# Kernel optimization log

Hardware: AMD Instinct MI355X
Metric: run time of the kernel (lower is better)

The kernel has to match this reference:

```python
import jax, jax.numpy as jnp
import numpy as np

N = 65536          # particles
E = 524288         # relations (avg degree 8)
RIG = 4096         # rigid instance = particles [0, RIG); fluid = [RIG, N)
PSTEPS = 2
ATTR, STATE, RELD, NF = 3, 6, 1, 128
DT = 1.0 / 60.0
MEAN_P = np.zeros(3, np.float32); STD_P = np.ones(3, np.float32)
MEAN_V = np.zeros(3, np.float32); STD_V = np.ones(3, np.float32)


def _lin(x, w, b):
    return x @ w.T + b  # torch Linear convention: w is [out, in]


def setup_inputs() -> dict:
    key = jax.random.key(0)
    ks = iter(jax.random.split(key, 40))
    d = {}
    d["state"] = jax.random.normal(next(ks), (N, STATE), jnp.float32)
    d["attr"] = jax.random.normal(next(ks), (N, ATTR), jnp.float32)
    d["Ra"] = jax.random.normal(next(ks), (E, RELD), jnp.float32)
    d["rel_recv"] = jax.random.randint(next(ks), (E,), 0, N, jnp.int32)
    d["rel_send"] = jax.random.randint(next(ks), (E,), 0, N, jnp.int32)

    def w(shape):
        return jax.random.normal(next(ks), shape, jnp.float32) / np.sqrt(shape[1])

    d["pe_w0"] = w((NF, ATTR + 2 * STATE)); d["pe_b0"] = jnp.zeros(NF)
    d["pe_w1"] = w((NF, NF)); d["pe_b1"] = jnp.zeros(NF)
    d["re_w0"] = w((NF, 2 * ATTR + 4 * STATE + RELD)); d["re_b0"] = jnp.zeros(NF)
    d["re_w1"] = w((NF, NF)); d["re_b1"] = jnp.zeros(NF)
    d["re_w2"] = w((NF, NF)); d["re_b2"] = jnp.zeros(NF)
    d["rp_w"] = w((NF, 3 * NF)); d["rp_b"] = jnp.zeros(NF)
    d["pp_w"] = w((NF, 2 * NF)); d["pp_b"] = jnp.zeros(NF)
    d["rg_w0"] = w((NF, NF)); d["rg_b0"] = jnp.zeros(NF)
    d["rg_w1"] = w((NF, NF)); d["rg_b1"] = jnp.zeros(NF)
    d["rg_w2"] = w((7, NF)); d["rg_b2"] = jnp.zeros(7)
    d["fl_w0"] = w((NF, NF)); d["fl_b0"] = jnp.zeros(NF)
    d["fl_w1"] = w((NF, NF)); d["fl_b1"] = jnp.zeros(NF)
    d["fl_w2"] = w((3, NF)); d["fl_b2"] = jnp.zeros(3)
    return d


def reference(state, attr, Ra, rel_recv, rel_send,
              pe_w0, pe_b0, pe_w1, pe_b1,
              re_w0, re_b0, re_w1, re_b1, re_w2, re_b2,
              rp_w, rp_b, pp_w, pp_b,
              rg_w0, rg_b0, rg_w1, rg_b1, rg_w2, rg_b2,
              fl_w0, fl_b0, fl_w1, fl_b1, fl_w2, fl_b2):
    relu = jax.nn.relu
    mean_p = jnp.asarray(MEAN_P); std_p = jnp.asarray(STD_P)
    mean_v = jnp.asarray(MEAN_V); std_v = jnp.asarray(STD_V)

    # rigid-body offset (state minus instance centroid for the rigid instance)
    offset = jnp.zeros_like(state).at[:RIG].set(
        state[:RIG] - jnp.mean(state[:RIG], axis=0))
    attr2 = jnp.concatenate([attr, offset], axis=1)        # [N, ATTR+STATE]

    # f_O^enc: particle encoder on [attr2, state]
    pe_in = jnp.concatenate([attr2, state], axis=1)         # [N, 15]
    particle_encode = relu(_lin(relu(_lin(pe_in, pe_w0, pe_b0)), pe_w1, pe_b1))

    # f_R^enc: relation encoder on gathered receiver/sender features
    rel_in = jnp.concatenate([attr2[rel_recv], attr2[rel_send],
                              state[rel_recv], state[rel_send], Ra], axis=1)  # [E, 31]
    h = relu(_lin(rel_in, re_w0, re_b0))
    h = relu(_lin(h, re_w1, re_b1))
    relation_encode = relu(_lin(h, re_w2, re_b2))           # [E, NF]

    # propagation: gather effects -> f_R -> scatter-add -> f_O
    effect = jnp.zeros((N, NF), state.dtype)
    for _ in range(PSTEPS):
        r_eff = effect[rel_recv]                            # [E, NF]
        s_eff = effect[rel_send]                            # [E, NF]
        rel_eff = relu(_lin(jnp.concatenate(
            [relation_encode, r_eff, s_eff], axis=1), rp_w, rp_b))
        agg = jax.ops.segment_sum(rel_eff, rel_recv, num_segments=N)  # Rr @ rel_eff
        effect = relu(_lin(jnp.concatenate(
            [particle_encode, agg], axis=1), pp_w, pp_b))   # residual=False

    # rigid predictor: quaternion + translation of the rigid body
    pooled = jnp.mean(effect[:RIG], axis=0)                 # [NF]
    t = _lin(relu(_lin(relu(_lin(pooled, rg_w0, rg_b0)), rg_w1, rg_b1)), rg_w2, rg_b2)
    q = t[:4] / jnp.linalg.norm(t[:4])
    w, x, y, z = q[0], q[1], q[2], q[3]
    R = jnp.stack([
        jnp.stack([1.0 - 2 * (y * y + z * z), 2 * (x * y + z * w), 2 * (x * z - y * w)]),
        jnp.stack([2 * (x * y - z * w), 1.0 - 2 * (x * x + z * z), 2 * (y * z + x * w)]),
        jnp.stack([2 * (x * z + y * w), 2 * (y * z - x * w), 1.0 - 2 * (x * x + y * y)]),
    ])
    b = t[4:] * std_p
    p0 = state[:RIG, :3] * std_p + mean_p
    c = jnp.mean(p0, axis=0)
    p1 = (p0 - c) @ R + b + c
    v = (p1 - p0) / DT
    pred_rigid = (v - mean_v) / std_v                       # [RIG, 3]

    # fluid predictor: per-particle MLP
    f = relu(_lin(effect[RIG:], fl_w0, fl_b0))
    f = relu(_lin(f, fl_w1, fl_b1))
    pred_fluid = _lin(f, fl_w2, fl_b2)                      # [N-RIG, 3]

    return jnp.concatenate([pred_rigid, pred_fluid], axis=0)  # [N, 3]
```

## Files before the change

kernel.cpp:

```cpp
#include <hip/hip_runtime.h>
#include <hip/hip_bf16.h>
#include <cstdio>

#define N_P   65536
#define N_E   524288
#define RIG_  4096

typedef __attribute__((ext_vector_type(8))) short bf16x8;
typedef __attribute__((ext_vector_type(4))) float f32x4;
typedef unsigned short u16;
typedef unsigned int   u32;

__device__ __forceinline__ u16 f2b(float x) {
    __hip_bfloat16 h = __float2bfloat16(x);
    return *(u16*)&h;
}
__device__ __forceinline__ float b2f(u16 u) {
    union { unsigned u; float f; } c; c.u = ((unsigned)u) << 16; return c.f;
}
__device__ __forceinline__ unsigned pk2(float x, float y) {
    return (unsigned)f2b(x) | ((unsigned)f2b(y) << 16);
}
#define MFMA(a,b,c) __builtin_amdgcn_mfma_f32_16x16x32_bf16((a),(b),(c),0,0,0)

__global__ __launch_bounds__(256) void k_hist(const int* __restrict__ recv,
                                              u32* __restrict__ cnt) {
    int i = blockIdx.x * 256 + threadIdx.x;
    if (i < N_E) atomicAdd(&cnt[recv[i]], 1u);
}
__global__ __launch_bounds__(256) void k_scan1(u32* __restrict__ data,
                                               u32* __restrict__ bsum) {
    __shared__ u32 s[256];
    int t = threadIdx.x, g = blockIdx.x * 256 + t;
    u32 v = data[g];
    s[t] = v; __syncthreads();
    for (int o = 1; o < 256; o <<= 1) {
        u32 x = (t >= o) ? s[t - o] : 0u;
        __syncthreads(); s[t] += x; __syncthreads();
    }
    data[g] = s[t] - v;
    if (t == 255) bsum[blockIdx.x] = s[255];
}
__global__ __launch_bounds__(256) void k_scan2(u32* __restrict__ bsum) {
    __shared__ u32 s[256];
    int t = threadIdx.x;
    u32 v = bsum[t];
    s[t] = v; __syncthreads();
    for (int o = 1; o < 256; o <<= 1) {
        u32 x = (t >= o) ? s[t - o] : 0u;
        __syncthreads(); s[t] += x; __syncthreads();
    }
    bsum[t] = s[t] - v;
}
__global__ __launch_bounds__(256) void k_scan3(u32* __restrict__ data,
                                               const u32* __restrict__ bsum) {
    int g = blockIdx.x * 256 + threadIdx.x;
    data[g] += bsum[blockIdx.x];
}
__global__ __launch_bounds__(256) void k_scatter(const int* __restrict__ recv,
                                                 const int* __restrict__ send,
                                                 u32* __restrict__ head,
                                                 u32* __restrict__ perm,
                                                 int* __restrict__ srecv,
                                                 int* __restrict__ ssend) {
    int i = blockIdx.x * 256 + threadIdx.x;
    if (i < N_E) {
        int n = recv[i];
        u32 pos = atomicAdd(&head[n], 1u);
        perm[pos] = (u32)i;
        srecv[pos] = n;
        ssend[pos] = send[i];
    }
}

struct CvtJob { const float* src; u16* dst; int n; int mode; int bstart; };
struct CvtArgs { CvtJob j[14]; };

__global__ __launch_bounds__(256) void k_cvt_all(CvtArgs a) {
    int b = blockIdx.x;
    int ji = 0;
    #pragma unroll
    for (int k = 1; k < 14; k++) if (b >= a.j[k].bstart) ji = k;
    CvtJob jb = a.j[ji];
    int i = (b - jb.bstart) * 256 + threadIdx.x;
    if (i >= jb.n) return;
    if (jb.mode == 0) {
        jb.dst[i] = f2b(jb.src[i]);
    } else if (jb.mode == 2) {
        int r = i >> 7;
        jb.dst[i] = (r < 3) ? f2b(jb.src[i]) : 0;
    } else if (jb.mode == 3) {
        int r = i >> 7, c = i & 127;
        jb.dst[i] = f2b(jb.src[r * 384 + c]);
    } else if (jb.mode == 4) {
        int r = i >> 7, c = i & 127;
        jb.dst[i] = f2b(jb.src[r * 256 + c]);
    } else if (jb.mode == 5) {
        int r = i >> 5, c = i & 31;
        float v = 0.f;
        if (c < 9)       v = jb.src[r * 31 + c];
        else if (c < 15) v = jb.src[r * 31 + 18 + (c - 9)];
        jb.dst[i] = f2b(v);
    } else if (jb.mode == 6) {
        int r = i >> 5, c = i & 31;
        float v = 0.f;
        if (c < 9)       v = jb.src[r * 31 + 9 + c];
        else if (c < 15) v = jb.src[r * 31 + 24 + (c - 9)];
        jb.dst[i] = f2b(v);
    } else {
        int r = i >> 5, c = i & 31;
        jb.dst[i] = (c < 15) ? f2b(jb.src[r * 15 + c]) : 0;
    }
}

__global__ __launch_bounds__(256) void k_centroid(const float* __restrict__ state,
                                                  float* __restrict__ cent) {
    int d = blockIdx.x;
    __shared__ float red[256];
    float s = 0.f;
    for (int r = threadIdx.x; r < RIG_; r += 256) s += state[r * 6 + d];
    red[threadIdx.x] = s; __syncthreads();
    for (int o = 128; o > 0; o >>= 1) {
        if (threadIdx.x < o) red[threadIdx.x] += red[threadIdx.x + o];
        __syncthreads();
    }
    if (threadIdx.x == 0) cent[d] = red[0] / (float)RIG_;
}

__global__ __launch_bounds__(256) void k_particle_ext(
        const float* __restrict__ state, const float* __restrict__ attr,
        const float* __restrict__ cent,
        const u16* __restrict__ w0r, const u16* __restrict__ w0s,
        const u16* __restrict__ pew0, const float* __restrict__ pe_b0,
        const u16* __restrict__ pew1, const float* __restrict__ pe_b1,
        const u16* __restrict__ wp,
        u16* __restrict__ P, u16* __restrict__ Q, u16* __restrict__ T) {
    __shared__ float in_s[64][16];
    __shared__ u16 INF[64 * 32];
    __shared__ __align__(16) u16 BUF[64 * 128];
    __shared__ float b0_s[128], b1_s[128];
    int t = threadIdx.x;
    int base = blockIdx.x * 64;
    if (t < 128) { b0_s[t] = pe_b0[t]; b1_s[t] = pe_b1[t]; }
    for (int it = t; it < 64 * 15; it += 256) {
        int r = it / 15, c = it % 15;
        int p = base + r;
        float v;
        if (c < 3)      v = attr[p * 3 + c];
        else if (c < 9) v = (p < RIG_) ? (state[p * 6 + (c - 3)] - cent[c - 3]) : 0.0f;
        else            v = state[p * 6 + (c - 9)];
        in_s[r][c] = v;
    }
    __syncthreads();
    int wv = t >> 6, kq4 = (t >> 4) & 3, m = t & 15;
    {
        int e = wv * 16 + m;
        u16 tmp[8];
        #pragma unroll
        for (int j = 0; j < 8; j++) {
            int k = kq4 * 8 + j;
            tmp[j] = (k < 15) ? f2b(in_s[e][k]) : (u16)0;
        }
        *(uint4*)&INF[((wv * 4 + kq4) * 16 + m) * 8] = *(uint4*)tmp;
    }
    int lane = t & 63, mm = lane & 15, quad = lane >> 4;
    bf16x8 af0 = *(const bf16x8*)&INF[((wv * 4 + quad) * 16 + mm) * 8];
    {
        f32x4 acc[8] = {};
        #pragma unroll
        for (int nt = 0; nt < 8; nt++) {
            bf16x8 bf = *(const bf16x8*)(w0r + (size_t)(nt * 16 + mm) * 32 + quad * 8);
            acc[nt] = MFMA(af0, bf, acc[nt]);
        }
        #pragma unroll
        for (int nt = 0; nt < 8; nt++) {
            int col = nt * 16 + mm;
            #pragma unroll
            for (int rg = 0; rg < 4; rg++) {
                int row = wv * 16 + quad * 4 + rg;
                P[(size_t)(base + row) * 128 + col] = f2b(acc[nt][rg]);
            }
        }
    }
    {
        f32x4 acc[8] = {};
        #pragma unroll
        for (int nt = 0; nt < 8; nt++) {
            bf16x8 bf = *(const bf16x8*)(w0s + (size_t)(nt * 16 + mm) * 32 + quad * 8);
            acc[nt] = MFMA(af0, bf, acc[nt]);
        }
        #pragma unroll
        for (int nt = 0; nt < 8; nt++) {
            int col = nt * 16 + mm;
            #pragma unroll
            for (int rg = 0; rg < 4; rg++) {
                int row = wv * 16 + quad * 4 + rg;
                Q[(size_t)(base + row) * 128 + col] = f2b(acc[nt][rg]);
            }
        }
    }
    {
        f32x4 acc[8] = {};
        #pragma unroll
        for (int nt = 0; nt < 8; nt++) {
            bf16x8 bf = *(const bf16x8*)(pew0 + (size_t)(nt * 16 + mm) * 32 + quad * 8);
            acc[nt] = MFMA(af0, bf, acc[nt]);
        }
        #pragma unroll
        for (int nt = 0; nt < 8; nt++) {
            int col = nt * 16 + mm;
            #pragma unroll
            for (int rg = 0; rg < 4; rg++) {
                BUF[((wv * 16 + (col >> 3)) * 16 + quad * 4 + rg) * 8 + (col & 7)] =
                    f2b(fmaxf(acc[nt][rg] + b0_s[col], 0.f));
            }
        }
    }
    {
        f32x4 acc[8] = {};
        for (int kc = 0; kc < 4; kc++) {
            bf16x8 af = *(const bf16x8*)&BUF[((wv * 16 + kc * 4 + quad) * 16 + mm) * 8];
            #pragma unroll
            for (int nt = 0; nt < 8; nt++) {
                bf16x8 bf = *(const bf16x8*)(pew1 + (size_t)(nt * 16 + mm) * 128 + kc * 32 + quad * 8);
                acc[nt] = MFMA(af, bf, acc[nt]);
            }
        }
        #pragma unroll
        for (int nt = 0; nt < 8; nt++) {
            int col = nt * 16 + mm;
            #pragma unroll
            for (int rg = 0; rg < 4; rg++) {
                BUF[((wv * 16 + (col >> 3)) * 16 + quad * 4 + rg) * 8 + (col & 7)] =
                    f2b(fmaxf(acc[nt][rg] + b1_s[col], 0.f));
            }
        }
    }
    {
        f32x4 acc[8] = {};
        for (int kc = 0; kc < 4; kc++) {
            bf16x8 af = *(const bf16x8*)&BUF[((wv * 16 + kc * 4 + quad) * 16 + mm) * 8];
            #pragma unroll
            for (int nt = 0; nt < 8; nt++) {
                bf16x8 bf = *(const bf16x8*)(wp + (size_t)(nt * 16 + mm) * 128 + kc * 32 + quad * 8);
                acc[nt] = MFMA(af, bf, acc[nt]);
            }
        }
        #pragma unroll
        for (int nt = 0; nt < 8; nt++) {
            int col = nt * 16 + mm;
            #pragma unroll
            for (int rg = 0; rg < 4; rg++) {
                int row = wv * 16 + quad * 4 + rg;
                T[(size_t)(base + row) * 128 + col] = f2b(acc[nt][rg]);
            }
        }
    }
}

__global__ __launch_bounds__(512, 4) void k_rel(
        const u16* __restrict__ P, const u16* __restrict__ Q,
        const float* __restrict__ Ra, const u32* __restrict__ perm,
        const int* __restrict__ srecv, const int* __restrict__ ssend,
        const float* __restrict__ re_w0_raw, const float* __restrict__ b0,
        const u16* __restrict__ w1b, const float* __restrict__ b1,
        const u16* __restrict__ w2b, const float* __restrict__ b2,
        const u16* __restrict__ wreb, const float* __restrict__ rpb,
        u16* __restrict__ Z, float* __restrict__ agg) {
    __shared__ __align__(16) u16 BUF[64 * 130];
    __shared__ int rv_s[64];
    __shared__ float wRa_s[128], b0_s[128];
    int t = threadIdx.x;
    if (t < 128) { wRa_s[t] = re_w0_raw[t * 31 + 30]; b0_s[t] = b0[t]; }
    int w = t >> 6, lane = t & 63, mm = lane & 15, quad = lane >> 4;
    int colw = w * 16 + mm;
    bf16x8 W1f[4], W2f[4], WEf[4];
    #pragma unroll
    for (int kc = 0; kc < 4; kc++) {
        W1f[kc] = *(const bf16x8*)(w1b  + (size_t)colw * 128 + kc * 32 + quad * 8);
        W2f[kc] = *(const bf16x8*)(w2b  + (size_t)colw * 128 + kc * 32 + quad * 8);
        WEf[kc] = *(const bf16x8*)(wreb + (size_t)colw * 128 + kc * 32 + quad * 8);
    }
    float b1c = b1[colw], b2c = b2[colw], rpbc = rpb[colw];
    int es = t >> 3, cs2 = (t & 7) * 2;
    int egs = es >> 4, ms = es & 15;
    int sseg = t >> 7, cseg = t & 127;

    for (long tile = blockIdx.x; tile < N_E / 64; tile += gridDim.x) {
        long base = tile * 64;
        __syncthreads();
        if (t < 64) rv_s[t] = srecv[base + t];
        {
            int rvp = srecv[base + es], svp = ssend[base + es];
            float ra = Ra[perm[base + es]];
            #pragma unroll
            for (int ci = 0; ci < 2; ci++) {
                int kq = cs2 + ci;
                uint4 up = *(const uint4*)(P + (size_t)rvp * 128 + kq * 8);
                uint4 uq = *(const uint4*)(Q + (size_t)svp * 128 + kq * 8);
                const u16* pp = (const u16*)&up; const u16* qq = (const u16*)&uq;
                u16 outv[8];
                #pragma unroll
                for (int j = 0; j < 8; j++) {
                    int c = kq * 8 + j;
                    float v = b2f(pp[j]) + b2f(qq[j]) + ra * wRa_s[c] + b0_s[c];
                    outv[j] = f2b(fmaxf(v, 0.f));
                }
                *(uint4*)&BUF[((egs * 16 + kq) * 16 + ms) * 8] = *(uint4*)outv;
            }
        }
        __syncthreads();
        {
            f32x4 acc[4] = {};
            #pragma unroll
            for (int eg = 0; eg < 4; eg++)
                #pragma unroll
                for (int kc = 0; kc < 4; kc++) {
                    bf16x8 af = *(const bf16x8*)&BUF[((eg * 16 + kc * 4 + quad) * 16 + mm) * 8];
                    acc[eg] = MFMA(af, W1f[kc], acc[eg]);
                }
            __syncthreads();
            #pragma unroll
            for (int eg = 0; eg < 4; eg++)
                #pragma unroll
                for (int rg = 0; rg < 4; rg++)
                    BUF[((eg * 16 + (colw >> 3)) * 16 + quad * 4 + rg) * 8 + (colw & 7)] =
                        f2b(fmaxf(acc[eg][rg] + b1c, 0.f));
        }
        __syncthreads();
        {
            f32x4 acc[4] = {};
            #pragma unroll
            for (int eg = 0; eg < 4; eg++)
                #pragma unroll
                for (int kc = 0; kc < 4; kc++) {
                    bf16x8 af = *(const bf16x8*)&BUF[((eg * 16 + kc * 4 + quad) * 16 + mm) * 8];
                    acc[eg] = MFMA(af, W2f[kc], acc[eg]);
                }
            __syncthreads();
            #pragma unroll
            for (int eg = 0; eg < 4; eg++)
                #pragma unroll
                for (int rg = 0; rg < 4; rg++)
                    BUF[((eg * 16 + (colw >> 3)) * 16 + quad * 4 + rg) * 8 + (colw & 7)] =
                        f2b(fmaxf(acc[eg][rg] + b2c, 0.f));
        }
        __syncthreads();
        {
            f32x4 zacc[4] = {};
            #pragma unroll
            for (int eg = 0; eg < 4; eg++)
                #pragma unroll
                for (int kc = 0; kc < 4; kc++) {
                    bf16x8 af = *(const bf16x8*)&BUF[((eg * 16 + kc * 4 + quad) * 16 + mm) * 8];
                    zacc[eg] = MFMA(af, WEf[kc], zacc[eg]);
                }
            #pragma unroll
            for (int eg = 0; eg < 4; eg++)
                #pragma unroll
                for (int rg = 0; rg < 4; rg++)
                    Z[(base + eg * 16 + quad * 4 + rg) * 128 + colw] = f2b(zacc[eg][rg]);
            __syncthreads();
            #pragma unroll
            for (int eg = 0; eg < 4; eg++)
                #pragma unroll
                for (int rg = 0; rg < 4; rg++)
                    BUF[(eg * 16 + quad * 4 + rg) * 130 + colw] =
                        f2b(fmaxf(zacc[eg][rg] + rpbc, 0.f));
        }
        __syncthreads();
        {
            int r0 = sseg * 16;
            int cur = rv_s[r0];
            float a = b2f(BUF[r0 * 130 + cseg]);
            for (int rr = r0 + 1; rr < r0 + 16; rr++) {
                int n = rv_s[rr];
                float v = b2f(BUF[rr * 130 + cseg]);
                if (n == cur) a += v;
                else { atomicAdd(&agg[(size_t)cur * 128 + cseg], a); cur = n; a = v; }
            }
            atomicAdd(&agg[(size_t)cur * 128 + cseg], a);
        }
    }
}

__global__ __launch_bounds__(256) void k_node2(
        const float* __restrict__ agg, const u16* __restrict__ T,
        const u16* __restrict__ wab, const float* __restrict__ ppb,
        u16* __restrict__ effb,
        const u16* __restrict__ wrb, const u16* __restrict__ wsb,
        u16* __restrict__ U, u16* __restrict__ V) {
    __shared__ __align__(16) u16 AF[64 * 128];
    int t = threadIdx.x;
    long base = (long)blockIdx.x * 64;
    int wv = t >> 6, kq4 = (t >> 4) & 3, m = t & 15;
    {
        long node = base + wv * 16 + m;
        #pragma unroll
        for (int i = 0; i < 4; i++) {
            int kq = kq4 + 4 * i;
            const float* src = agg + node * 128 + kq * 8;
            float4 f0 = *(const float4*)src, f1 = *(const float4*)(src + 4);
            uint4 v;
            v.x = pk2(f0.x, f0.y); v.y = pk2(f0.z, f0.w);
            v.z = pk2(f1.x, f1.y); v.w = pk2(f1.z, f1.w);
            *(uint4*)&AF[((wv * 16 + kq) * 16 + m) * 8] = v;
        }
    }
    int lane = t & 63, mm = lane & 15, quad = lane >> 4;
    f32x4 acc[8] = {};
    for (int kc = 0; kc < 4; kc++) {
        bf16x8 af = *(const bf16x8*)&AF[((wv * 16 + kc * 4 + quad) * 16 + mm) * 8];
        #pragma unroll
        for (int nt = 0; nt < 8; nt++) {
            bf16x8 bf = *(const bf16x8*)(wab + (size_t)(nt * 16 + mm) * 128 + kc * 32 + quad * 8);
            acc[nt] = MFMA(af, bf, acc[nt]);
        }
    }
    #pragma unroll
    for (int nt = 0; nt < 8; nt++) {
        int col = nt * 16 + mm;
        #pragma unroll
        for (int rg = 0; rg < 4; rg++) {
            long row = base + wv * 16 + quad * 4 + rg;
            float v = acc[nt][rg] + b2f(T[row * 128 + col]) + ppb[col];
            u16 e = f2b(fmaxf(v, 0.f));
            effb[row * 128 + col] = e;
            if (U)
                AF[((wv * 16 + (col >> 3)) * 16 + quad * 4 + rg) * 8 + (col & 7)] = e;
        }
    }
    if (U) {
        {
            f32x4 au[8] = {};
            for (int kc = 0; kc < 4; kc++) {
                bf16x8 af = *(const bf16x8*)&AF[((wv * 16 + kc * 4 + quad) * 16 + mm) * 8];
                #pragma unroll
                for (int nt = 0; nt < 8; nt++) {
                    bf16x8 bu = *(const bf16x8*)(wrb + (size_t)(nt * 16 + mm) * 128 + kc * 32 + quad * 8);
                    au[nt] = MFMA(af, bu, au[nt]);
                }
            }
            #pragma unroll
            for (int nt = 0; nt < 8; nt++) {
                int col = nt * 16 + mm;
                #pragma unroll
                for (int rg = 0; rg < 4; rg++) {
                    long row = base + wv * 16 + quad * 4 + rg;
                    U[row * 128 + col] = f2b(au[nt][rg]);
                }
            }
        }
        {
            f32x4 av[8] = {};
            for (int kc = 0; kc < 4; kc++) {
                bf16x8 af = *(const bf16x8*)&AF[((wv * 16 + kc * 4 + quad) * 16 + mm) * 8];
                #pragma unroll
                for (int nt = 0; nt < 8; nt++) {
                    bf16x8 bv = *(const bf16x8*)(wsb + (size_t)(nt * 16 + mm) * 128 + kc * 32 + quad * 8);
                    av[nt] = MFMA(af, bv, av[nt]);
                }
            }
            #pragma unroll
            for (int nt = 0; nt < 8; nt++) {
                int col = nt * 16 + mm;
                #pragma unroll
                for (int rg = 0; rg < 4; rg++) {
                    long row = base + wv * 16 + quad * 4 + rg;
                    V[row * 128 + col] = f2b(av[nt][rg]);
                }
            }
        }
    }
}

__global__ __launch_bounds__(256) void k_edge2(
        const u16* __restrict__ Z, const u16* __restrict__ U, const u16* __restrict__ V,
        const int* __restrict__ srecv, const int* __restrict__ ssend,
        const float* __restrict__ rpb, float* __restrict__ agg) {
    __shared__ __align__(16) u16 S16[64 * 136];
    __shared__ int rv_s[64];
    __shared__ float rpb_s[128];
    int t = threadIdx.x;
    long base = (long)blockIdx.x * 64;
    if (t < 64) rv_s[t] = srecv[base + t];
    if (t < 128) rpb_s[t] = rpb[t];
    int r = t >> 2, q = t & 3;
    int rv = srecv[base + r];
    int sv = ssend[base + r];
    long zb = (base + r) * 128;
    size_t ub = (size_t)rv * 128, vb = (size_t)sv * 128;
    __syncthreads();
    #pragma unroll
    for (int i = 0; i < 4; i++) {
        int c0 = q * 32 + i * 8;
        uint4 uz = *(const uint4*)(Z + zb + c0);
        uint4 uu = *(const uint4*)(U + ub + c0);
        uint4 uv = *(const uint4*)(V + vb + c0);
        const u16* zz = (const u16*)&uz; const u16* pu = (const u16*)&uu; const u16* pv = (const u16*)&uv;
        u16 o[8];
        #pragma unroll
        for (int j = 0; j < 8; j++)
            o[j] = f2b(fmaxf(b2f(zz[j]) + b2f(pu[j]) + b2f(pv[j]) + rpb_s[c0 + j], 0.f));
        *(uint4*)&S16[r * 136 + c0] = *(uint4*)o;
    }
    __syncthreads();
    {
        int s = t >> 7, col = t & 127;
        int r0 = s * 32;
        int cur = rv_s[r0];
        float a = b2f(S16[r0 * 136 + col]);
        for (int rr = r0 + 1; rr < r0 + 32; rr++) {
            int n = rv_s[rr];
            float v = b2f(S16[rr * 136 + col]);
            if (n == cur) a += v;
            else { atomicAdd(&agg[(size_t)cur * 128 + col], a); cur = n; a = v; }
        }
        atomicAdd(&agg[(size_t)cur * 128 + col], a);
    }
}

__global__ __launch_bounds__(256) void k_pool(const u16* __restrict__ effb,
                                              float* __restrict__ pooled) {
    int f = blockIdx.x;
    __shared__ float red[256];
    float s = 0.f;
    for (int r = threadIdx.x; r < RIG_; r += 256) s += b2f(effb[(size_t)r * 128 + f]);
    red[threadIdx.x] = s; __syncthreads();
    for (int o = 128; o > 0; o >>= 1) {
        if (threadIdx.x < o) red[threadIdx.x] += red[threadIdx.x + o];
        __syncthreads();
    }
    if (threadIdx.x == 0) pooled[f] = red[0] / (float)RIG_;
}

__global__ __launch_bounds__(128) void k_rigid_head(
        const float* __restrict__ pooled,
        const float* __restrict__ w0, const float* __restrict__ b0,
        const float* __restrict__ w1, const float* __restrict__ b1,
        const float* __restrict__ w2, const float* __restrict__ b2,
        float* __restrict__ rig) {
    __shared__ float pl[128], ha[128], hb[128], tv[7];
    int t = threadIdx.x;
    pl[t] = pooled[t];
    __syncthreads();
    float a = b0[t];
    for (int k = 0; k < 128; k++) a += w0[t * 128 + k] * pl[k];
    ha[t] = fmaxf(a, 0.f);
    __syncthreads();
    a = b1[t];
    for (int k = 0; k < 128; k++) a += w1[t * 128 + k] * ha[k];
    hb[t] = fmaxf(a, 0.f);
    __syncthreads();
    if (t < 7) {
        float s = b2[t];
        for (int k = 0; k < 128; k++) s += w2[t * 128 + k] * hb[k];
        tv[t] = s;
    }
    __syncthreads();
    if (t == 0) {
        float w = tv[0], x = tv[1], y = tv[2], z = tv[3];
        float n = sqrtf(w * w + x * x + y * y + z * z);
        w /= n; x /= n; y /= n; z /= n;
        rig[0] = 1.f - 2.f * (y * y + z * z); rig[1] = 2.f * (x * y + z * w); rig[2] = 2.f * (x * z - y * w);
        rig[3] = 2.f * (x * y - z * w); rig[4] = 1.f - 2.f * (x * x + z * z); rig[5] = 2.f * (y * z + x * w);
        rig[6] = 2.f * (x * z + y * w); rig[7] = 2.f * (y * z - x * w); rig[8] = 1.f - 2.f * (x * x + y * y);
        rig[9] = tv[4]; rig[10] = tv[5]; rig[11] = tv[6];
    }
}

__global__ __launch_bounds__(256) void k_rigid_out(
        const float* __restrict__ state, const float* __restrict__ cent,
        const float* __restrict__ rig, float* __restrict__ out) {
    int i = blockIdx.x * 256 + threadIdx.x;
    if (i >= RIG_) return;
    float p0[3], d[3];
    #pragma unroll
    for (int k = 0; k < 3; k++) { p0[k] = state[i * 6 + k]; d[k] = p0[k] - cent[k]; }
    #pragma unroll
    for (int j = 0; j < 3; j++) {
        float p1 = rig[0 * 3 + j] * d[0] + rig[1 * 3 + j] * d[1] + rig[2 * 3 + j] * d[2]
                 + rig[9 + j] + cent[j];
        out[i * 3 + j] = (p1 - p0[j]) * 60.0f;
    }
}

#define HPAD 136
__global__ __launch_bounds__(256) void k_fluid(
        const u16* __restrict__ effb,
        const u16* __restrict__ w0b, const float* __restrict__ b0,
        const u16* __restrict__ w1b, const float* __restrict__ b1,
        const u16* __restrict__ w2b, const float* __restrict__ b2,
        float* __restrict__ out) {
    __shared__ __align__(16) u16 H[64 * HPAD];
    int t = threadIdx.x;
    long base = RIG_ + (long)blockIdx.x * 64;
    int r = t >> 2, q = t & 3;
    {
        const u16* src = effb + (base + r) * 128 + q * 32;
        u16* dst = &H[r * HPAD + q * 32];
        #pragma unroll
        for (int i = 0; i < 32; i += 8)
            *(uint4*)(dst + i) = *(const uint4*)(src + i);
    }
    int wv = t >> 6, lane = t & 63;
    int m = lane & 15, quad = lane >> 4;
    {
        f32x4 acc[8] = {};
        for (int kc = 0; kc < 4; kc++) {
            bf16x8 af = *(const bf16x8*)&H[(wv * 16 + m) * HPAD + kc * 32 + quad * 8];
            #pragma unroll
            for (int nt = 0; nt < 8; nt++) {
                bf16x8 bf = *(const bf16x8*)(w0b + (size_t)(nt * 16 + m) * 128 + kc * 32 + quad * 8);
                acc[nt] = MFMA(af, bf, acc[nt]);
            }
        }
        #pragma unroll
        for (int nt = 0; nt < 8; nt++) {
            int col = nt * 16 + m;
            float bv = b0[col];
            #pragma unroll
            for (int rg = 0; rg < 4; rg++) {
                int row = wv * 16 + quad * 4 + rg;
                H[row * HPAD + col] = f2b(fmaxf(acc[nt][rg] + bv, 0.f));
            }
        }
    }
    {
        f32x4 acc[8] = {};
        for (int kc = 0; kc < 4; kc++) {
            bf16x8 af = *(const bf16x8*)&H[(wv * 16 + m) * HPAD + kc * 32 + quad * 8];
            #pragma unroll
            for (int nt = 0; nt < 8; nt++) {
                bf16x8 bf = *(const bf16x8*)(w1b + (size_t)(nt * 16 + m) * 128 + kc * 32 + quad * 8);
                acc[nt] = MFMA(af, bf, acc[nt]);
            }
        }
        #pragma unroll
        for (int nt = 0; nt < 8; nt++) {
            int col = nt * 16 + m;
            float bv = b1[col];
            #pragma unroll
            for (int rg = 0; rg < 4; rg++) {
                int row = wv * 16 + quad * 4 + rg;
                H[row * HPAD + col] = f2b(fmaxf(acc[nt][rg] + bv, 0.f));
            }
        }
    }
    {
        f32x4 acc = {};
        for (int kc = 0; kc < 4; kc++) {
            bf16x8 af = *(const bf16x8*)&H[(wv * 16 + m) * HPAD + kc * 32 + quad * 8];
            bf16x8 bf = *(const bf16x8*)(w2b + (size_t)m * 128 + kc * 32 + quad * 8);
            acc = MFMA(af, bf, acc);
        }
        if (m < 3) {
            float bv = b2[m];
            #pragma unroll
            for (int rg = 0; rg < 4; rg++) {
                long row = base + wv * 16 + quad * 4 + rg;
                out[row * 3 + m] = acc[rg] + bv;
            }
        }
    }
}

extern "C" void kernel_launch(void* const* d_in, const int* in_sizes, int n_in,
                              void* d_out, int out_size, void* d_ws, size_t ws_size,
                              hipStream_t stream) {
    const float* state = (const float*)d_in[0];
    const float* attr  = (const float*)d_in[1];
    const float* Ra    = (const float*)d_in[2];
    const int*   recv  = (const int*)d_in[3];
    const int*   send  = (const int*)d_in[4];
    const float* pe_w0 = (const float*)d_in[5];  const float* pe_b0 = (const float*)d_in[6];
    const float* pe_w1 = (const float*)d_in[7];  const float* pe_b1 = (const float*)d_in[8];
    const float* re_w0 = (const float*)d_in[9];  const float* re_b0 = (const float*)d_in[10];
    const float* re_w1 = (const float*)d_in[11]; const float* re_b1 = (const float*)d_in[12];
    const float* re_w2 = (const float*)d_in[13]; const float* re_b2 = (const float*)d_in[14];
    const float* rp_w  = (const float*)d_in[15]; const float* rp_b  = (const float*)d_in[16];
    const float* pp_w  = (const float*)d_in[17]; const float* pp_b  = (const float*)d_in[18];
    const float* rg_w0 = (const float*)d_in[19]; const float* rg_b0 = (const float*)d_in[20];
    const float* rg_w1 = (const float*)d_in[21]; const float* rg_b1 = (const float*)d_in[22];
    const float* rg_w2 = (const float*)d_in[23]; const float* rg_b2 = (const float*)d_in[24];
    const float* fl_w0 = (const float*)d_in[25]; const float* fl_b0 = (const float*)d_in[26];
    const float* fl_w1 = (const float*)d_in[27]; const float* fl_b1 = (const float*)d_in[28];
    const float* fl_w2 = (const float*)d_in[29]; const float* fl_b2 = (const float*)d_in[30];
    float* out = (float*)d_out;

    char* p = (char*)d_ws;
    auto alloc = [&](size_t bytes) { char* r = p; p += (bytes + 255) / 256 * 256; return r; };
    float* cent    = (float*)alloc(8 * 4);
    float* pooled  = (float*)alloc(128 * 4);
    float* rig     = (float*)alloc(16 * 4);
    u32*   rowhead = (u32*)alloc((size_t)N_P * 4);
    u32*   bsum    = (u32*)alloc(256 * 4);
    u32*   perm    = (u32*)alloc((size_t)N_E * 4);
    int*   srecv   = (int*)alloc((size_t)N_E * 4);
    int*   ssend   = (int*)alloc((size_t)N_E * 4);
    float* agg     = (float*)alloc((size_t)N_P * 128 * 4);
    u16*   Z       = (u16*)alloc((size_t)N_E * 128 * 2);
    u16*   effb    = (u16*)alloc((size_t)N_P * 128 * 2);
    u16*   T       = (u16*)alloc((size_t)N_P * 128 * 2);
    u16*   P       = (u16*)alloc((size_t)N_P * 128 * 2);
    u16*   Q       = (u16*)alloc((size_t)N_P * 128 * 2);
    u16*   wreb    = (u16*)alloc(128 * 128 * 2);
    u16*   wrb     = (u16*)alloc(128 * 128 * 2);
    u16*   wsb     = (u16*)alloc(128 * 128 * 2);
    u16*   wpb     = (u16*)alloc(128 * 128 * 2);
    u16*   wab     = (u16*)alloc(128 * 128 * 2);
    u16*   rw1b    = (u16*)alloc(128 * 128 * 2);
    u16*   rw2b    = (u16*)alloc(128 * 128 * 2);
    u16*   pew1b   = (u16*)alloc(128 * 128 * 2);
    u16*   flw0b   = (u16*)alloc(128 * 128 * 2);
    u16*   flw1b   = (u16*)alloc(128 * 128 * 2);
    u16*   flw2b   = (u16*)alloc(16 * 128 * 2);
    u16*   w0rb    = (u16*)alloc(128 * 32 * 2);
    u16*   w0sb    = (u16*)alloc(128 * 32 * 2);
    u16*   pew0b   = (u16*)alloc(128 * 32 * 2);
    size_t need = (size_t)(p - (char*)d_ws);
    if (ws_size < need) {
        fprintf(stderr, "kernel_launch: ws_size %zu < needed %zu\n", ws_size, need);
        return;
    }
    u16* U = P; u16* V = Q;

    hipMemsetAsync(rowhead, 0, (size_t)N_P * 4, stream);
    k_hist<<<N_E / 256, 256, 0, stream>>>(recv, rowhead);
    k_scan1<<<N_P / 256, 256, 0, stream>>>(rowhead, bsum);
    k_scan2<<<1, 256, 0, stream>>>(bsum);
    k_scan3<<<N_P / 256, 256, 0, stream>>>(rowhead, bsum);
    k_scatter<<<N_E / 256, 256, 0, stream>>>(recv, send, rowhead, perm, srecv, ssend);

    CvtArgs ca;
    int bs = 0;
    auto addjob = [&](int idx, const float* s, u16* d, int n, int mode) {
        ca.j[idx] = {s, d, n, mode, bs};
        bs += (n + 255) / 256;
    };
    addjob(0,  rp_w,        wreb,  128 * 128, 3);
    addjob(1,  rp_w + 128,  wrb,   128 * 128, 3);
    addjob(2,  rp_w + 256,  wsb,   128 * 128, 3);
    addjob(3,  pp_w,        wpb,   128 * 128, 4);
    addjob(4,  pp_w + 128,  wab,   128 * 128, 4);
    addjob(5,  re_w1,       rw1b,  128 * 128, 0);
    addjob(6,  re_w2,       rw2b,  128 * 128, 0);
    addjob(7,  pe_w1,       pew1b, 128 * 128, 0);
    addjob(8,  fl_w0,       flw0b, 128 * 128, 0);
    addjob(9,  fl_w1,       flw1b, 128 * 128, 0);
    addjob(10, fl_w2,       flw2b, 16 * 128,  2);
    addjob(11, re_w0,       w0rb,  128 * 32,  5);
    addjob(12, re_w0,       w0sb,  128 * 32,  6);
    addjob(13, pe_w0,       pew0b, 128 * 32,  7);
    k_cvt_all<<<bs, 256, 0, stream>>>(ca);

    k_centroid<<<6, 256, 0, stream>>>(state, cent);
    k_particle_ext<<<N_P / 64, 256, 0, stream>>>(state, attr, cent,
                                                 w0rb, w0sb, pew0b, pe_b0,
                                                 pew1b, pe_b1, wpb, P, Q, T);

    hipMemsetAsync(agg, 0, (size_t)N_P * 128 * 4, stream);
    k_rel<<<512, 512, 0, stream>>>(P, Q, Ra, perm, srecv, ssend,
                                   re_w0, re_b0, rw1b, re_b1, rw2b, re_b2,
                                   wreb, rp_b, Z, agg);
    k_node2<<<N_P / 64, 256, 0, stream>>>(agg, T, wab, pp_b, effb, wrb, wsb, U, V);

    hipMemsetAsync(agg, 0, (size_t)N_P * 128 * 4, stream);
    k_edge2<<<N_E / 64, 256, 0, stream>>>(Z, U, V, srecv, ssend, rp_b, agg);
    k_node2<<<N_P / 64, 256, 0, stream>>>(agg, T, wab, pp_b, effb,
                                          nullptr, nullptr, nullptr, nullptr);

    k_pool<<<128, 256, 0, stream>>>(effb, pooled);
    k_rigid_head<<<1, 128, 0, stream>>>(pooled, rg_w0, rg_b0, rg_w1, rg_b1, rg_w2, rg_b2, rig);
    k_rigid_out<<<(RIG_ + 255) / 256, 256, 0, stream>>>(state, cent, rig, out);
    k_fluid<<<(N_P - RIG_) / 64, 256, 0, stream>>>(effb, flw0b, fl_b0, flw1b, fl_b1,
                                                   flw2b, fl_b2, out);
}
```

Measured before the change: 568.5 us.

## Fuse fluid MLP into final node update and replace interior segment atomics with stores

```diff
diff --git a/kernel.cpp b/kernel.cpp
--- a/kernel.cpp
+++ b/kernel.cpp
@@ -373,11 +373,16 @@
             int r0 = sseg * 16;
             int cur = rv_s[r0];
             float a = b2f(BUF[r0 * 130 + cseg]);
+            bool first = true;
             for (int rr = r0 + 1; rr < r0 + 16; rr++) {
                 int n = rv_s[rr];
                 float v = b2f(BUF[rr * 130 + cseg]);
                 if (n == cur) a += v;
-                else { atomicAdd(&agg[(size_t)cur * 128 + cseg], a); cur = n; a = v; }
+                else {
+                    if (first) atomicAdd(&agg[(size_t)cur * 128 + cseg], a);
+                    else       agg[(size_t)cur * 128 + cseg] = a;
+                    first = false; cur = n; a = v;
+                }
             }
             atomicAdd(&agg[(size_t)cur * 128 + cseg], a);
         }
@@ -425,50 +430,168 @@
             long row = base + wv * 16 + quad * 4 + rg;
             float v = acc[nt][rg] + b2f(T[row * 128 + col]) + ppb[col];
             u16 e = f2b(fmaxf(v, 0.f));
-            effb[row * 128 + col] = e;
-            if (U)
-                AF[((wv * 16 + (col >> 3)) * 16 + quad * 4 + rg) * 8 + (col & 7)] = e;
-        }
-    }
-    if (U) {
-        {
-            f32x4 au[8] = {};
-            for (int kc = 0; kc < 4; kc++) {
-                bf16x8 af = *(const bf16x8*)&AF[((wv * 16 + kc * 4 + quad) * 16 + mm) * 8];
-                #pragma unroll
-                for (int nt = 0; nt < 8; nt++) {
-                    bf16x8 bu = *(const bf16x8*)(wrb + (size_t)(nt * 16 + mm) * 128 + kc * 32 + quad * 8);
-                    au[nt] = MFMA(af, bu, au[nt]);
-                }
-            }
+            if (effb) effb[row * 128 + col] = e;
+            AF[((wv * 16 + (col >> 3)) * 16 + quad * 4 + rg) * 8 + (col & 7)] = e;
+        }
+    }
+    {
+        f32x4 au[8] = {};
+        for (int kc = 0; kc < 4; kc++) {
+            bf16x8 af = *(const bf16x8*)&AF[((wv * 16 + kc * 4 + quad) * 16 + mm) * 8];
             #pragma unroll
             for (int nt = 0; nt < 8; nt++) {
-                int col = nt * 16 + mm;
-                #pragma unroll
-                for (int rg = 0; rg < 4; rg++) {
-                    long row = base + wv * 16 + quad * 4 + rg;
-                    U[row * 128 + col] = f2b(au[nt][rg]);
-                }
-            }
-        }
-        {
-            f32x4 av[8] = {};
-            for (int kc = 0; kc < 4; kc++) {
-                bf16x8 af = *(const bf16x8*)&AF[((wv * 16 + kc * 4 + quad) * 16 + mm) * 8];
-                #pragma unroll
-                for (int nt = 0; nt < 8; nt++) {
-                    bf16x8 bv = *(const bf16x8*)(wsb + (size_t)(nt * 16 + mm) * 128 + kc * 32 + quad * 8);
-                    av[nt] = MFMA(af, bv, av[nt]);
-                }
-            }
+                bf16x8 bu = *(const bf16x8*)(wrb + (size_t)(nt * 16 + mm) * 128 + kc * 32 + quad * 8);
+                au[nt] = MFMA(af, bu, au[nt]);
+            }
+        }
+        #pragma unroll
+        for (int nt = 0; nt < 8; nt++) {
+            int col = nt * 16 + mm;
+            #pragma unroll
+            for (int rg = 0; rg < 4; rg++) {
+                long row = base + wv * 16 + quad * 4 + rg;
+                U[row * 128 + col] = f2b(au[nt][rg]);
+            }
+        }
+    }
+    {
+        f32x4 av[8] = {};
+        for (int kc = 0; kc < 4; kc++) {
+            bf16x8 af = *(const bf16x8*)&AF[((wv * 16 + kc * 4 + quad) * 16 + mm) * 8];
             #pragma unroll
             for (int nt = 0; nt < 8; nt++) {
-                int col = nt * 16 + mm;
-                #pragma unroll
-                for (int rg = 0; rg < 4; rg++) {
-                    long row = base + wv * 16 + quad * 4 + rg;
-                    V[row * 128 + col] = f2b(av[nt][rg]);
-                }
+                bf16x8 bv = *(const bf16x8*)(wsb + (size_t)(nt * 16 + mm) * 128 + kc * 32 + quad * 8);
+                av[nt] = MFMA(af, bv, av[nt]);
+            }
+        }
+        #pragma unroll
+        for (int nt = 0; nt < 8; nt++) {
+            int col = nt * 16 + mm;
+            #pragma unroll
+            for (int rg = 0; rg < 4; rg++) {
+                long row = base + wv * 16 + quad * 4 + rg;
+                V[row * 128 + col] = f2b(av[nt][rg]);
+            }
+        }
+    }
+}
+
+#define HPAD 136
+__global__ __launch_bounds__(256) void k_node2fl(
+        const float* __restrict__ agg, const u16* __restrict__ T,
+        const u16* __restrict__ wab, const float* __restrict__ ppb,
+        u16* __restrict__ effb,
+        const u16* __restrict__ w0b, const float* __restrict__ b0,
+        const u16* __restrict__ w1b, const float* __restrict__ b1,
+        const u16* __restrict__ w2b, const float* __restrict__ b2,
+        float* __restrict__ out) {
+    __shared__ __align__(16) u16 H[64 * HPAD];
+    int t = threadIdx.x;
+    long base = (long)blockIdx.x * 64;
+    bool fluid = (base >= RIG_);
+    int wv = t >> 6, kq4 = (t >> 4) & 3, m = t & 15;
+    {
+        long node = base + wv * 16 + m;
+        #pragma unroll
+        for (int i = 0; i < 4; i++) {
+            int kq = kq4 + 4 * i;
+            const float* src = agg + node * 128 + kq * 8;
+            float4 f0 = *(const float4*)src, f1 = *(const float4*)(src + 4);
+            uint4 v;
+            v.x = pk2(f0.x, f0.y); v.y = pk2(f0.z, f0.w);
+            v.z = pk2(f1.x, f1.y); v.w = pk2(f1.z, f1.w);
+            *(uint4*)&H[((wv * 16 + kq) * 16 + m) * 8] = v;
+        }
+    }
+    int lane = t & 63, mm = lane & 15, quad = lane >> 4;
+    f32x4 acc[8] = {};
+    for (int kc = 0; kc < 4; kc++) {
+        bf16x8 af = *(const bf16x8*)&H[((wv * 16 + kc * 4 + quad) * 16 + mm) * 8];
+        #pragma unroll
+        for (int nt = 0; nt < 8; nt++) {
+            bf16x8 bf = *(const bf16x8*)(wab + (size_t)(nt * 16 + mm) * 128 + kc * 32 + quad * 8);
+            acc[nt] = MFMA(af, bf, acc[nt]);
+        }
+    }
+    if (!fluid) {
+        #pragma unroll
+        for (int nt = 0; nt < 8; nt++) {
+            int col = nt * 16 + mm;
+            #pragma unroll
+            for (int rg = 0; rg < 4; rg++) {
+                long row = base + wv * 16 + quad * 4 + rg;
+                float v = acc[nt][rg] + b2f(T[row * 128 + col]) + ppb[col];
+                effb[row * 128 + col] = f2b(fmaxf(v, 0.f));
+            }
+        }
+        return;
+    }
+    __syncthreads();
+    #pragma unroll
+    for (int nt = 0; nt < 8; nt++) {
+        int col = nt * 16 + mm;
+        #pragma unroll
+        for (int rg = 0; rg < 4; rg++) {
+            long row = base + wv * 16 + quad * 4 + rg;
+            float v = acc[nt][rg] + b2f(T[row * 128 + col]) + ppb[col];
+            H[(wv * 16 + quad * 4 + rg) * HPAD + col] = f2b(fmaxf(v, 0.f));
+        }
+    }
+    {
+        f32x4 a8[8] = {};
+        for (int kc = 0; kc < 4; kc++) {
+            bf16x8 af = *(const bf16x8*)&H[(wv * 16 + mm) * HPAD + kc * 32 + quad * 8];
+            #pragma unroll
+            for (int nt = 0; nt < 8; nt++) {
+                bf16x8 bf = *(const bf16x8*)(w0b + (size_t)(nt * 16 + mm) * 128 + kc * 32 + quad * 8);
+                a8[nt] = MFMA(af, bf, a8[nt]);
+            }
+        }
+        #pragma unroll
+        for (int nt = 0; nt < 8; nt++) {
+            int col = nt * 16 + mm;
+            float bv = b0[col];
+            #pragma unroll
+            for (int rg = 0; rg < 4; rg++) {
+                int row = wv * 16 + quad * 4 + rg;
+                H[row * HPAD + col] = f2b(fmaxf(a8[nt][rg] + bv, 0.f));
+            }
+        }
+    }
+    {
+        f32x4 a8[8] = {};
+        for (int kc = 0; kc < 4; kc++) {
+            bf16x8 af = *(const bf16x8*)&H[(wv * 16 + mm) * HPAD + kc * 32 + quad * 8];
+            #pragma unroll
+            for (int nt = 0; nt < 8; nt++) {
+                bf16x8 bf = *(const bf16x8*)(w1b + (size_t)(nt * 16 + mm) * 128 + kc * 32 + quad * 8);
+                a8[nt] = MFMA(af, bf, a8[nt]);
+            }
+        }
+        #pragma unroll
+        for (int nt = 0; nt < 8; nt++) {
+            int col = nt * 16 + mm;
+            float bv = b1[col];
+            #pragma unroll
+            for (int rg = 0; rg < 4; rg++) {
+                int row = wv * 16 + quad * 4 + rg;
+                H[row * HPAD + col] = f2b(fmaxf(a8[nt][rg] + bv, 0.f));
+            }
+        }
+    }
+    {
+        f32x4 a1 = {};
+        for (int kc = 0; kc < 4; kc++) {
+            bf16x8 af = *(const bf16x8*)&H[(wv * 16 + mm) * HPAD + kc * 32 + quad * 8];
+            bf16x8 bf = *(const bf16x8*)(w2b + (size_t)mm * 128 + kc * 32 + quad * 8);
+            a1 = MFMA(af, bf, a1);
+        }
+        if (mm < 3) {
+            float bv = b2[mm];
+            #pragma unroll
+            for (int rg = 0; rg < 4; rg++) {
+                long row = base + wv * 16 + quad * 4 + rg;
+                out[row * 3 + mm] = a1[rg] + bv;
             }
         }
     }
@@ -510,11 +633,16 @@
         int r0 = s * 32;
         int cur = rv_s[r0];
         float a = b2f(S16[r0 * 136 + col]);
+        bool first = true;
         for (int rr = r0 + 1; rr < r0 + 32; rr++) {
             int n = rv_s[rr];
             float v = b2f(S16[rr * 136 + col]);
             if (n == cur) a += v;
-            else { atomicAdd(&agg[(size_t)cur * 128 + col], a); cur = n; a = v; }
+            else {
+                if (first) atomicAdd(&agg[(size_t)cur * 128 + col], a);
+                else       agg[(size_t)cur * 128 + col] = a;
+                first = false; cur = n; a = v;
+            }
         }
         atomicAdd(&agg[(size_t)cur * 128 + col], a);
     }
@@ -582,86 +710,6 @@
         float p1 = rig[0 * 3 + j] * d[0] + rig[1 * 3 + j] * d[1] + rig[2 * 3 + j] * d[2]
                  + rig[9 + j] + cent[j];
         out[i * 3 + j] = (p1 - p0[j]) * 60.0f;
-    }
-}
-
-#define HPAD 136
-__global__ __launch_bounds__(256) void k_fluid(
-        const u16* __restrict__ effb,
-        const u16* __restrict__ w0b, const float* __restrict__ b0,
-        const u16* __restrict__ w1b, const float* __restrict__ b1,
-        const u16* __restrict__ w2b, const float* __restrict__ b2,
-        float* __restrict__ out) {
-    __shared__ __align__(16) u16 H[64 * HPAD];
-    int t = threadIdx.x;
-    long base = RIG_ + (long)blockIdx.x * 64;
-    int r = t >> 2, q = t & 3;
-    {
-        const u16* src = effb + (base + r) * 128 + q * 32;
-        u16* dst = &H[r * HPAD + q * 32];
-        #pragma unroll
-        for (int i = 0; i < 32; i += 8)
-            *(uint4*)(dst + i) = *(const uint4*)(src + i);
-    }
-    int wv = t >> 6, lane = t & 63;
-    int m = lane & 15, quad = lane >> 4;
-    {
-        f32x4 acc[8] = {};
-        for (int kc = 0; kc < 4; kc++) {
-            bf16x8 af = *(const bf16x8*)&H[(wv * 16 + m) * HPAD + kc * 32 + quad * 8];
-            #pragma unroll
-            for (int nt = 0; nt < 8; nt++) {
-                bf16x8 bf = *(const bf16x8*)(w0b + (size_t)(nt * 16 + m) * 128 + kc * 32 + quad * 8);
-                acc[nt] = MFMA(af, bf, acc[nt]);
-            }
-        }
-        #pragma unroll
-        for (int nt = 0; nt < 8; nt++) {
-            int col = nt * 16 + m;
-            float bv = b0[col];
-            #pragma unroll
-            for (int rg = 0; rg < 4; rg++) {
-                int row = wv * 16 + quad * 4 + rg;
-                H[row * HPAD + col] = f2b(fmaxf(acc[nt][rg] + bv, 0.f));
-            }
-        }
-    }
-    {
-        f32x4 acc[8] = {};
-        for (int kc = 0; kc < 4; kc++) {
-            bf16x8 af = *(const bf16x8*)&H[(wv * 16 + m) * HPAD + kc * 32 + quad * 8];
-            #pragma unroll
-            for (int nt = 0; nt < 8; nt++) {
-                bf16x8 bf = *(const bf16x8*)(w1b + (size_t)(nt * 16 + m) * 128 + kc * 32 + quad * 8);
-                acc[nt] = MFMA(af, bf, acc[nt]);
-            }
-        }
-        #pragma unroll
-        for (int nt = 0; nt < 8; nt++) {
-            int col = nt * 16 + m;
-            float bv = b1[col];
-            #pragma unroll
-            for (int rg = 0; rg < 4; rg++) {
-                int row = wv * 16 + quad * 4 + rg;
-                H[row * HPAD + col] = f2b(fmaxf(acc[nt][rg] + bv, 0.f));
-            }
-        }
-    }
-    {
-        f32x4 acc = {};
-        for (int kc = 0; kc < 4; kc++) {
-            bf16x8 af = *(const bf16x8*)&H[(wv * 16 + m) * HPAD + kc * 32 + quad * 8];
-            bf16x8 bf = *(const bf16x8*)(w2b + (size_t)m * 128 + kc * 32 + quad * 8);
-            acc = MFMA(af, bf, acc);
-        }
-        if (m < 3) {
-            float bv = b2[m];
-            #pragma unroll
-            for (int rg = 0; rg < 4; rg++) {
-                long row = base + wv * 16 + quad * 4 + rg;
-                out[row * 3 + m] = acc[rg] + bv;
-            }
-        }
     }
 }
 
@@ -760,19 +808,18 @@
                                                  pew1b, pe_b1, wpb, P, Q, T);
 
     hipMemsetAsync(agg, 0, (size_t)N_P * 128 * 4, stream);
-    k_rel<<<512, 512, 0, stream>>>(P, Q, Ra, perm, srecv, ssend,
-                                   re_w0, re_b0, rw1b, re_b1, rw2b, re_b2,
-                                   wreb, rp_b, Z, agg);
-    k_node2<<<N_P / 64, 256, 0, stream>>>(agg, T, wab, pp_b, effb, wrb, wsb, U, V);
+    k_rel<<<1024, 512, 0, stream>>>(P, Q, Ra, perm, srecv, ssend,
+                                    re_w0, re_b0, rw1b, re_b1, rw2b, re_b2,
+                                    wreb, rp_b, Z, agg);
+    k_node2<<<N_P / 64, 256, 0, stream>>>(agg, T, wab, pp_b, nullptr, wrb, wsb, U, V);
 
     hipMemsetAsync(agg, 0, (size_t)N_P * 128 * 4, stream);
     k_edge2<<<N_E / 64, 256, 0, stream>>>(Z, U, V, srecv, ssend, rp_b, agg);
-    k_node2<<<N_P / 64, 256, 0, stream>>>(agg, T, wab, pp_b, effb,
-                                          nullptr, nullptr, nullptr, nullptr);
+    k_node2fl<<<N_P / 64, 256, 0, stream>>>(agg, T, wab, pp_b, effb,
+                                            flw0b, fl_b0, flw1b, fl_b1,
+                                            flw2b, fl_b2, out);
 
     k_pool<<<128, 256, 0, stream>>>(effb, pooled);
     k_rigid_head<<<1, 128, 0, stream>>>(pooled, rg_w0, rg_b0, rg_w1, rg_b1, rg_w2, rg_b2, rig);
     k_rigid_out<<<(RIG_ + 255) / 256, 256, 0, stream>>>(state, cent, rig, out);
-    k_fluid<<<(N_P - RIG_) / 64, 256, 0, stream>>>(effb, flw0b, fl_b0, flw1b, fl_b1,
-                                                   flw2b, fl_b2, out);
-}
+}
```

After: 579.8 us. No clear change (+2.0%).
